# Optimization experiments

Measured on AMD Instinct MI355X. Metric: run time of the kernel, lower is better.

The kernel has to match this reference:

```python
import jax, jax.numpy as jnp
import numpy as np

N, K, C = 32768, 64, 256
PAIR, HID, BINS, CLIP = 32, 64, 16, 32
LN_EPS = 1e-5


def setup_inputs() -> dict:
    key = jax.random.key(0)
    ks = jax.random.split(key, 12)
    inp = {
        "features": jax.random.normal(ks[0], (N, C), jnp.float32),
        "resi": jnp.arange(N, dtype=jnp.int32),
        "chain": jax.random.randint(ks[1], (N,), 0, 4, jnp.int32),
        "batch": jax.random.randint(ks[2], (N,), 0, 8, jnp.int32),
        "neighbours": jax.random.randint(ks[3], (N, K), 0, N, jnp.int32),
        # learned params
        "W_left": jax.random.normal(ks[4], (C, PAIR), jnp.float32) / np.sqrt(C),
        "W_right": jax.random.normal(ks[5], (C, PAIR), jnp.float32) / np.sqrt(C),
        "W_pos": jax.random.normal(ks[6], (2 * CLIP + 1, PAIR), jnp.float32) * 0.1,
        "ln_scale": jnp.ones((PAIR,), jnp.float32),
        "ln_bias": jnp.zeros((PAIR,), jnp.float32),
        "W1": jax.random.normal(ks[7], (PAIR, HID), jnp.float32) / np.sqrt(PAIR),
        "b1": jnp.zeros((HID,), jnp.float32),
        "W2": jax.random.normal(ks[8], (HID, BINS), jnp.float32) / np.sqrt(HID),
        "b2": jnp.zeros((BINS,), jnp.float32),
    }
    return inp


def reference(features, resi, chain, batch, neighbours,
              W_left, W_right, W_pos, ln_scale, ln_bias, W1, b1, W2, b2):
    # left/right 32-dim codes, pairwise combine via neighbour gather: [N,K,32]
    left = features @ W_left
    right = features @ W_right
    dcode = left[:, None, :] + right[neighbours]

    # relative sequence position one-hot (65 classes) -> Linear(32, bias=False).
    # one_hot @ W_pos == row-gather of W_pos; masked to same chain & batch.
    rel = jnp.clip(resi[neighbours] - resi[:, None], -CLIP, CLIP) + CLIP  # [N,K]
    same = (chain[neighbours] == chain[:, None]) & (batch[neighbours] == batch[:, None])
    dcode = dcode + jnp.where(same[..., None], W_pos[rel], 0.0)

    # LayerNorm over last axis (scale + offset)
    mu = dcode.mean(-1, keepdims=True)
    var = jnp.mean(jnp.square(dcode - mu), -1, keepdims=True)
    dcode = (dcode - mu) * jax.lax.rsqrt(var + LN_EPS) * ln_scale + ln_bias

    # 2-layer GELU MLP -> 16 bins
    h = jax.nn.gelu(dcode @ W1 + b1)
    logits = h @ W2 + b2
    log_p = jax.nn.log_softmax(logits, axis=-1)

    # softmax-weighted expected distance over bin centers of [0, 22) A
    step = 22.0 / BINS
    bin_centers = (jnp.arange(BINS, dtype=jnp.float32) + 0.5) * step
    dmap = (jnp.exp(log_p) * bin_centers).sum(axis=-1)  # [N,K]
    return log_p, dmap
```

## Files before the change

kernel.cpp:

```cpp
#include <hip/hip_runtime.h>
#include <stdint.h>

#define N_RES 32768
#define KNEI  64
#define CFEAT 256
#define PAIRD 32
#define HIDD  64
#define NBINS 16
#define CLIPV 32
#define NPAIRS (N_RES * KNEI)
#define NGROUPS (NPAIRS / 16)

typedef __attribute__((ext_vector_type(2))) _Float16 half2_t;
typedef __attribute__((ext_vector_type(8))) _Float16 half8_t;
typedef __attribute__((ext_vector_type(2))) __fp16   fp16v2;
typedef __attribute__((ext_vector_type(4))) float    float4_t;

union H2U { uint32_t u; half2_t h; fp16v2 f; };
union V4H { uint4 v; uint32_t u[4]; half2_t h2[4]; };
union V8H { uint32_t u[4]; half2_t h2[4]; half8_t h8; };

__device__ __forceinline__ uint32_t pkh(float a, float b) {
    H2U c; c.f = __builtin_amdgcn_cvt_pkrtz(a, b);
    return c.u;
}
__device__ __forceinline__ half2_t pkh2(float a, float b) {
    H2U c; c.f = __builtin_amdgcn_cvt_pkrtz(a, b);
    return c.h;
}

__device__ __forceinline__ float fastrcp(float x) { return __builtin_amdgcn_rcpf(x); }
__device__ __forceinline__ float fexp2(float x)   { return __builtin_amdgcn_exp2f(x); }
__device__ __forceinline__ float flog2(float x)   { return __builtin_amdgcn_logf(x); }

__device__ __forceinline__ uint32_t addph(uint32_t a, uint32_t b) {
    H2U x, y; x.u = a; y.u = b; x.h = x.h + y.h; return x.u;
}

__device__ __forceinline__ half2_t gelu2(half2_t x) {
    const half2_t kA1  = {(_Float16)0.79788456f, (_Float16)0.79788456f};
    const half2_t kA2  = {(_Float16)0.035677408f,(_Float16)0.035677408f};
    const half2_t kPA1 = {(_Float16)2.0512820f,  (_Float16)2.0512820f};
    const half2_t kPA2 = {(_Float16)0.7160840f,  (_Float16)0.7160840f};
    const half2_t kPA3 = {(_Float16)0.0303104f,  (_Float16)0.0303104f};
    const half2_t kPB1 = {(_Float16)7.3846154f,  (_Float16)7.3846154f};
    const half2_t kPB2 = {(_Float16)5.9673660f,  (_Float16)5.9673660f};
    const half2_t kPB3 = {(_Float16)0.8486920f,  (_Float16)0.8486920f};
    const half2_t kOne = {(_Float16)1.0f,  (_Float16)1.0f};
    const half2_t kTwo = {(_Float16)2.0f,  (_Float16)2.0f};
    const half2_t kQtr = {(_Float16)0.25f, (_Float16)0.25f};
    const half2_t kHlf = {(_Float16)0.5f,  (_Float16)0.5f};
    const half2_t kClp = {(_Float16)4.5f,  (_Float16)4.5f};
    const half2_t kNCl = {(_Float16)-4.5f, (_Float16)-4.5f};

    half2_t u0 = x * x;
    half2_t y  = x * __builtin_elementwise_fma(kA2, u0, kA1);
    y = __builtin_elementwise_min(__builtin_elementwise_max(y, kNCl), kClp);
    half2_t yq = y * kQtr;
    half2_t v  = yq * yq;
    half2_t pa = __builtin_elementwise_fma(kPA3, v, kPA2);
    pa = __builtin_elementwise_fma(pa, v, kPA1);
    pa = __builtin_elementwise_fma(pa, v, kOne);
    half2_t pb = __builtin_elementwise_fma(kPB3, v, kPB2);
    pb = __builtin_elementwise_fma(pb, v, kPB1);
    pb = __builtin_elementwise_fma(pb, v, kOne);
    half2_t a = y * pa;
    H2U cb, cr;
    cb.h = pb;
    cr.u = 0x78007800u - cb.u;
    half2_t r = cr.h;
    r = r * __builtin_elementwise_fma(-pb, r, kTwo);
    r = r * __builtin_elementwise_fma(-pb, r, kTwo);
    half2_t th = a * r;
    half2_t hx = x * kHlf;
    return __builtin_elementwise_fma(hx, th, hx);
}

__global__ __launch_bounds__(256) void proj_kernel(
    const float* __restrict__ feat, const float* __restrict__ Wl,
    const float* __restrict__ Wr, const int* __restrict__ resi,
    const int* __restrict__ chain, const int* __restrict__ batch,
    const float* __restrict__ wpos,
    uint4* __restrict__ leftbf, uint4* __restrict__ rightbf,
    uint32_t* __restrict__ meta, uint32_t* __restrict__ wposbf)
{
    __shared__ __align__(16) float Wc[CFEAT * 32];
    const int tid   = threadIdx.x;
    const int half  = blockIdx.x >> 9;
    const int rb    = (blockIdx.x & 511) * 64;
    const float* W  = half ? Wr : Wl;
    uint4* outtb    = half ? rightbf : leftbf;

    for (int idx = tid; idx < CFEAT * 32; idx += 256)
        Wc[idx] = W[idx];
    if (half == 0 && tid < 64) {
        int r = rb + tid;
        meta[r] = (uint32_t)resi[r] | ((uint32_t)chain[r] << 16)
                | ((uint32_t)batch[r] << 19);
    }
    if (blockIdx.x == 0) {
        for (int i = tid; i < (2 * CLIPV + 1) * PAIRD / 2; i += 256)
            wposbf[i] = pkh(wpos[2 * i], wpos[2 * i + 1]);
    }
    __syncthreads();

    const int cb  = (tid & 3) * 8;
    const int row = rb + (tid >> 2);

    float acc[8];
#pragma unroll
    for (int j = 0; j < 8; ++j) acc[j] = 0.f;

    for (int i = 0; i < CFEAT; i += 4) {
        float4_t f = *(const float4_t*)(feat + (size_t)row * CFEAT + i);
#pragma unroll
        for (int s = 0; s < 4; ++s) {
            float4_t wa = *(const float4_t*)(Wc + (i + s) * 32 + cb);
            float4_t wb = *(const float4_t*)(Wc + (i + s) * 32 + cb + 4);
#pragma unroll
            for (int j = 0; j < 4; ++j) {
                acc[j]     = __builtin_fmaf(f[s], wa[j], acc[j]);
                acc[4 + j] = __builtin_fmaf(f[s], wb[j], acc[4 + j]);
            }
        }
    }
    uint2 o, o2;
    o.x  = pkh(acc[0], acc[1]);
    o.y  = pkh(acc[2], acc[3]);
    o2.x = pkh(acc[4], acc[5]);
    o2.y = pkh(acc[6], acc[7]);
    uint2* dst = (uint2*)outtb + (size_t)row * 8 + (cb >> 2);
    dst[0] = o;
    dst[1] = o2;
}

__global__ __launch_bounds__(256) void prepass_kernel(
    const int* __restrict__ nbr, const uint32_t* __restrict__ meta,
    unsigned char* __restrict__ rs)
{
    const int p  = blockIdx.x * 256 + threadIdx.x;
    const int nb = __builtin_nontemporal_load(nbr + p);
    const uint32_t mn = meta[p >> 6];
    const uint32_t mb = meta[nb];
    const int rel = min(max((int)(mb & 0xFFFFu) - (int)(mn & 0xFFFFu),
                            -CLIPV), CLIPV) + CLIPV;
    const unsigned int same = (((mb ^ mn) & 0xFFFF0000u) == 0u) ? 0x80u : 0u;
    __builtin_nontemporal_store((unsigned char)(rel | same), rs + p);
}

__global__ __launch_bounds__(256, 8) void pair_kernel(
    const uint4* __restrict__ leftbf, const uint4* __restrict__ rightbf,
    const unsigned char* __restrict__ rs, const int* __restrict__ nbr,
    const uint32_t* __restrict__ wposbf,
    const float* __restrict__ lnS, const float* __restrict__ lnB,
    const float* __restrict__ W1, const float* __restrict__ b1,
    const float* __restrict__ W2, const float* __restrict__ b2,
    float* __restrict__ out_logp, float* __restrict__ out_dmap)
{
    __shared__ __align__(16) unsigned char Hbuf[4][16 * 144];
    __shared__ __align__(16) float b1p[HIDD];

    const int tid    = threadIdx.x;
    const int lane   = tid & 63;
    const int wlocal = tid >> 6;
    const int q      = lane >> 4;
    const int c      = lane & 15;

    if (tid < HIDD) {
        float s = b1[tid];
        for (int k = 0; k < PAIRD; ++k)
            s = __builtin_fmaf(lnB[k], W1[k * HIDD + tid], s);
        b1p[tid] = s;
    }

    half8_t w1a[4];
#pragma unroll
    for (int t = 0; t < 4; ++t) {
        V8H tmp;
#pragma unroll
        for (int v = 0; v < 4; ++v) {
            int k0 = q * 8 + 2 * v, k1 = k0 + 1;
            float a0 = lnS[k0] * W1[k0 * HIDD + 16 * t + c];
            float a1 = lnS[k1] * W1[k1 * HIDD + 16 * t + c];
            tmp.u[v] = pkh(a0, a1);
        }
        w1a[t] = tmp.h8;
    }
    half8_t w2a[2];
#pragma unroll
    for (int kt = 0; kt < 2; ++kt) {
        V8H tmp;
#pragma unroll
        for (int v = 0; v < 4; ++v) {
            int k0 = kt * 32 + q * 8 + 2 * v;
            tmp.u[v] = pkh(W2[k0 * NBINS + c], W2[(k0 + 1) * NBINS + c]);
        }
        w2a[kt] = tmp.h8;
    }
    const float4_t b2f = *(const float4_t*)(b2 + 4 * q);

    __syncthreads();

    const int wglobal = (blockIdx.x * 256 + tid) >> 6;
    const int nwaves  = (gridDim.x * 256) >> 6;

    for (int g = wglobal; g < NGROUPS; g += nwaves) {
        const int pbase = g * 16;
        const int n = pbase >> 6;
        const int p = pbase + c;

        const int nb = __builtin_nontemporal_load(nbr + p);
        const unsigned int rsb = __builtin_nontemporal_load(rs + p);
        const uint4 lf = leftbf [(size_t)n  * 4 + q];
        const uint4 rf = rightbf[(size_t)nb * 4 + q];

        const int rel = rsb & 0x7Fu;
        const uint32_t mskbits = (rsb & 0x80u) ? 0x3C003C00u : 0u;
        const uint4 pw = *(const uint4*)(wposbf + rel * 16 + q * 4);

        V4H lu, ru, pu; lu.v = lf; ru.v = rf; pu.v = pw;
        H2U mm; mm.u = mskbits;
        const half2_t m2 = mm.h;
        half2_t d2[4];
#pragma unroll
        for (int v = 0; v < 4; ++v)
            d2[v] = __builtin_elementwise_fma(pu.h2[v], m2, lu.h2[v] + ru.h2[v]);

        half2_t a1 = (d2[0] + d2[1]) + (d2[2] + d2[3]);
        half2_t aq = __builtin_elementwise_fma(d2[0], d2[0],
                     __builtin_elementwise_fma(d2[1], d2[1],
                     __builtin_elementwise_fma(d2[2], d2[2], d2[3] * d2[3])));
        H2U c1, c2; c1.h = a1; c2.h = aq;
        uint32_t s1p = c1.u, s2p = c2.u;
        s1p = addph(s1p, (uint32_t)__shfl_xor((int)s1p, 16, 64));
        s1p = addph(s1p, (uint32_t)__shfl_xor((int)s1p, 32, 64));
        s2p = addph(s2p, (uint32_t)__shfl_xor((int)s2p, 16, 64));
        s2p = addph(s2p, (uint32_t)__shfl_xor((int)s2p, 32, 64));
        H2U f1, f2; f1.u = s1p; f2.u = s2p;
        const float s1 = (float)f1.h[0] + (float)f1.h[1];
        const float s2 = (float)f2.h[0] + (float)f2.h[1];
        const float mu   = s1 * (1.0f / 32.0f);
        const float var  = __builtin_fmaf(-mu, mu, s2 * (1.0f / 32.0f));
        const float rstd = __builtin_amdgcn_rsqf(var + 1e-5f);
        const float sh   = -mu * rstd;

        const half2_t rs2 = pkh2(rstd, rstd);
        const half2_t sh2 = pkh2(sh, sh);
        V8H dn;
#pragma unroll
        for (int v = 0; v < 4; ++v)
            dn.h2[v] = __builtin_elementwise_fma(d2[v], rs2, sh2);
        const half8_t dfrag = dn.h8;

        float4_t hacc[4];
#pragma unroll
        for (int t = 0; t < 4; ++t) {
            float4_t c1v = *(const float4_t*)(b1p + 16 * t + 4 * q);
            hacc[t] = __builtin_amdgcn_mfma_f32_16x16x32_f16(w1a[t], dfrag, c1v, 0, 0, 0);
        }

        unsigned char* hb = &Hbuf[wlocal][0] + c * 144;
#pragma unroll
        for (int t = 0; t < 4; ++t) {
            half2_t g01 = gelu2(pkh2(hacc[t][0], hacc[t][1]));
            half2_t g23 = gelu2(pkh2(hacc[t][2], hacc[t][3]));
            union { half2_t h[2]; uint2 u2; } w;
            w.h[0] = g01; w.h[1] = g23;
            *(uint2*)(hb + 32 * t + 8 * q) = w.u2;
        }
        const half8_t hf0 = *(const half8_t*)(hb + 16 * q);
        const half8_t hf1 = *(const half8_t*)(hb + 64 + 16 * q);

        float4_t lacc;
        lacc = __builtin_amdgcn_mfma_f32_16x16x32_f16(w2a[0], hf0, b2f,  0, 0, 0);
        lacc = __builtin_amdgcn_mfma_f32_16x16x32_f16(w2a[1], hf1, lacc, 0, 0, 0);

        const float LOG2E = 1.4426950408889634f, LN2 = 0.6931471805599453f;
        float e[4];
#pragma unroll
        for (int r = 0; r < 4; ++r) e[r] = fexp2(lacc[r] * LOG2E);
        float ssum = (e[0] + e[1]) + (e[2] + e[3]);
        ssum += __shfl_xor(ssum, 16, 64);
        ssum += __shfl_xor(ssum, 32, 64);
        const float lse = flog2(ssum) * LN2;

        float4_t lp = {lacc[0] - lse, lacc[1] - lse, lacc[2] - lse, lacc[3] - lse};
        __builtin_nontemporal_store(lp, (float4_t*)(out_logp + (size_t)p * NBINS + 4 * q));

        const float step  = 22.0f / NBINS;
        const float cbase = (4 * q + 0.5f) * step;
        float dpart = e[0] * cbase + e[1] * (cbase + step)
                    + e[2] * (cbase + 2 * step) + e[3] * (cbase + 3 * step);
        dpart += __shfl_xor(dpart, 16, 64);
        dpart += __shfl_xor(dpart, 32, 64);
        if (q == 0)
            __builtin_nontemporal_store(dpart * fastrcp(ssum), out_dmap + p);
    }
}

extern "C" void kernel_launch(void* const* d_in, const int* in_sizes, int n_in,
                              void* d_out, int out_size, void* d_ws, size_t ws_size,
                              hipStream_t stream) {
    const float* features = (const float*)d_in[0];
    const int*   resi     = (const int*)d_in[1];
    const int*   chain    = (const int*)d_in[2];
    const int*   batch    = (const int*)d_in[3];
    const int*   nbr      = (const int*)d_in[4];
    const float* W_left   = (const float*)d_in[5];
    const float* W_right  = (const float*)d_in[6];
    const float* W_pos    = (const float*)d_in[7];
    const float* ln_scale = (const float*)d_in[8];
    const float* ln_bias  = (const float*)d_in[9];
    const float* W1       = (const float*)d_in[10];
    const float* b1       = (const float*)d_in[11];
    const float* W2       = (const float*)d_in[12];
    const float* b2       = (const float*)d_in[13];

    char* ws = (char*)d_ws;
    uint4*         leftbf  = (uint4*)ws;
    uint4*         rightbf = (uint4*)(ws + (size_t)N_RES * 64);
    uint32_t*      meta    = (uint32_t*)(ws + (size_t)2 * N_RES * 64);
    uint32_t*      wposbf  = (uint32_t*)(ws + (size_t)2 * N_RES * 64 + N_RES * 4);
    unsigned char* rs      = (unsigned char*)(ws + (size_t)2 * N_RES * 64
                                              + N_RES * 4 + 8192);

    float* out_logp = (float*)d_out;
    float* out_dmap = out_logp + (size_t)N_RES * KNEI * NBINS;

    proj_kernel<<<1024, 256, 0, stream>>>(features, W_left, W_right,
                                          resi, chain, batch, W_pos,
                                          leftbf, rightbf, meta, wposbf);
    prepass_kernel<<<NPAIRS / 256, 256, 0, stream>>>(nbr, meta, rs);
    pair_kernel<<<2048, 256, 0, stream>>>(leftbf, rightbf, rs, nbr, wposbf,
                                          ln_scale, ln_bias, W1, b1, W2, b2,
                                          out_logp, out_dmap);
}
```

Baseline: 334.1 us.

## Process one residue per wave iteration with batched neighbour gathers

The wave loop now works on one residue per iteration instead of one 16-pair group. It loads all 64 neighbour indices and packed rel/mask words in a single coalesced load and spreads them with lane shuffles. It also issues the four right-feature gathers up front before processing the four groups, and loads the left feature once per residue. The aim is more memory-level parallelism and fewer small scattered index loads, at the cost of higher register pressure and coarser load balance across waves.

Result: slower. 441.6 us (+32.2%).

```diff
diff --git a/kernel.cpp b/kernel.cpp
--- a/kernel.cpp
+++ b/kernel.cpp
@@ -9,7 +9,6 @@
 #define NBINS 16
 #define CLIPV 32
 #define NPAIRS (N_RES * KNEI)
-#define NGROUPS (NPAIRS / 16)
 
 typedef __attribute__((ext_vector_type(2))) _Float16 half2_t;
 typedef __attribute__((ext_vector_type(8))) _Float16 half8_t;
@@ -201,25 +200,12 @@
 
     __syncthreads();
 
-    const int wglobal = (blockIdx.x * 256 + tid) >> 6;
-    const int nwaves  = (gridDim.x * 256) >> 6;
-
-    for (int g = wglobal; g < NGROUPS; g += nwaves) {
-        const int pbase = g * 16;
-        const int n = pbase >> 6;
-        const int p = pbase + c;
-
-        const int nb = __builtin_nontemporal_load(nbr + p);
-        const unsigned int rsb = __builtin_nontemporal_load(rs + p);
-        const uint4 lf = leftbf [(size_t)n  * 4 + q];
-        const uint4 rf = rightbf[(size_t)nb * 4 + q];
-
-        const int rel = rsb & 0x7Fu;
-        const uint32_t mskbits = (rsb & 0x80u) ? 0x3C003C00u : 0u;
-        const uint4 pw = *(const uint4*)(wposbf + rel * 16 + q * 4);
-
-        V4H lu, ru, pu; lu.v = lf; ru.v = rf; pu.v = pw;
-        H2U mm; mm.u = mskbits;
+    unsigned char* const hb = &Hbuf[wlocal][0] + c * 144;
+
+    auto process = [&](uint4 lfv, uint4 rfv, unsigned int rsb, int p) {
+        const uint4 pwv = *(const uint4*)(wposbf + (rsb & 0x7Fu) * 16 + q * 4);
+        V4H lu, ru, pu; lu.v = lfv; ru.v = rfv; pu.v = pwv;
+        H2U mm; mm.u = (rsb & 0x80u) ? 0x3C003C00u : 0u;
         const half2_t m2 = mm.h;
         half2_t d2[4];
 #pragma unroll
@@ -259,7 +245,6 @@
             hacc[t] = __builtin_amdgcn_mfma_f32_16x16x32_f16(w1a[t], dfrag, c1v, 0, 0, 0);
         }
 
-        unsigned char* hb = &Hbuf[wlocal][0] + c * 144;
 #pragma unroll
         for (int t = 0; t < 4; ++t) {
             half2_t g01 = gelu2(pkh2(hacc[t][0], hacc[t][1]));
@@ -295,6 +280,36 @@
         dpart += __shfl_xor(dpart, 32, 64);
         if (q == 0)
             __builtin_nontemporal_store(dpart * fastrcp(ssum), out_dmap + p);
+    };
+
+    const int wglobal = (blockIdx.x * 256 + tid) >> 6;
+    const int nwaves  = (gridDim.x * 256) >> 6;
+
+    for (int n = wglobal; n < N_RES; n += nwaves) {
+        const int base = n * KNEI;
+
+        const int          nbAll = nbr[base + lane];
+        const unsigned int rsAll = rs[base + lane];
+        const uint4        lf    = leftbf[(size_t)n * 4 + q];
+
+        const int nb0 = __shfl(nbAll, 0 * 16 + c, 64);
+        const int nb1 = __shfl(nbAll, 1 * 16 + c, 64);
+        const int nb2 = __shfl(nbAll, 2 * 16 + c, 64);
+        const int nb3 = __shfl(nbAll, 3 * 16 + c, 64);
+        const unsigned int rs0 = (unsigned int)__shfl((int)rsAll, 0 * 16 + c, 64);
+        const unsigned int rs1 = (unsigned int)__shfl((int)rsAll, 1 * 16 + c, 64);
+        const unsigned int rs2_ = (unsigned int)__shfl((int)rsAll, 2 * 16 + c, 64);
+        const unsigned int rs3 = (unsigned int)__shfl((int)rsAll, 3 * 16 + c, 64);
+
+        const uint4 rf0 = rightbf[(size_t)nb0 * 4 + q];
+        const uint4 rf1 = rightbf[(size_t)nb1 * 4 + q];
+        const uint4 rf2 = rightbf[(size_t)nb2 * 4 + q];
+        const uint4 rf3 = rightbf[(size_t)nb3 * 4 + q];
+
+        process(lf, rf0, rs0,  base +  0 + c);
+        process(lf, rf1, rs1,  base + 16 + c);
+        process(lf, rf2, rs2_, base + 32 + c);
+        process(lf, rf3, rs3,  base + 48 + c);
     }
 }
 
```
